# Performance work log

Hardware: AMD Instinct MI355X
Metric: run time of the kernel (lower is better)

The kernel has to match this reference:

```python
import jax, jax.numpy as jnp
import numpy as np

HIDDEN = 2048
HEADS = 16
HEAD_DIM = HIDDEN // HEADS


def setup_inputs() -> dict:
    key = jax.random.key(0)
    k1, k2, k3, k4, k5 = jax.random.split(key, 5)
    scale = 1.0 / np.sqrt(HIDDEN)
    x = jax.random.normal(k1, (2, 2048, HIDDEN), dtype=jnp.float32)
    # nn.Linear weights stored as [out_features, in_features]
    w_q = jax.random.normal(k2, (HIDDEN, HIDDEN), dtype=jnp.float32) * scale
    w_k = jax.random.normal(k3, (HEAD_DIM, HIDDEN), dtype=jnp.float32) * scale
    w_v = jax.random.normal(k4, (HEAD_DIM, HIDDEN), dtype=jnp.float32) * scale
    w_out = jax.random.normal(k5, (HIDDEN, HIDDEN), dtype=jnp.float32) * scale
    return {"x": x, "w_q": w_q, "w_k": w_k, "w_v": w_v, "w_out": w_out}


def reference(x, w_q, w_k, w_v, w_out) -> jnp.ndarray:
    bsz, seq_len, _ = x.shape
    norm = jnp.asarray(np.sqrt(HEAD_DIM), dtype=x.dtype)
    # projections (Linear: x @ W^T)
    q = (x @ w_q.T).reshape(bsz, seq_len, HEADS, HEAD_DIM)  # [b,s,h,d]
    k = x @ w_k.T  # [b,s,d] single shared KV head
    v = x @ w_v.T  # [b,s,d]
    # attention scores: [b,h,s,s], K/V broadcast across heads
    att = jnp.einsum("bshd,btd->bhst", q, k) / norm
    att = jax.nn.softmax(att, axis=-1)
    out = jnp.einsum("bhst,btd->bshd", att, v).reshape(bsz, seq_len, HIDDEN)
    return out @ w_out.T
```

## Files before the change

kernel.cpp:

```cpp
#include <hip/hip_runtime.h>


using bf16   = __bf16;
using bf16x2 = __bf16 __attribute__((ext_vector_type(2)));
using bf16x4 = __bf16 __attribute__((ext_vector_type(4)));
using bf16x8 = __bf16 __attribute__((ext_vector_type(8)));
using f32x4  = float  __attribute__((ext_vector_type(4)));
using u32x4  = unsigned __attribute__((ext_vector_type(4)));

#define GAS __attribute__((address_space(1)))
#define LAS __attribute__((address_space(3)))

__device__ __forceinline__ void load_lds16(const bf16* g, bf16* l) {
    __builtin_amdgcn_global_load_lds((const GAS void*)g, (LAS void*)l, 16, 0, 0);
}

__device__ __forceinline__ unsigned pkbf(float a, float b) {
    bf16x2 t; t[0] = (bf16)a; t[1] = (bf16)b;
    return __builtin_bit_cast(unsigned, t);
}
__device__ __forceinline__ void perm32(unsigned& a, unsigned& b) {
    asm volatile("v_permlane32_swap_b32 %0, %1" : "+v"(a), "+v"(b));
}
__device__ __forceinline__ void perm16(unsigned& a, unsigned& b) {
    asm volatile("v_permlane16_swap_b32 %0, %1" : "+v"(a), "+v"(b));
}

#define Q_SCALE_LOG2 0.12751745f

__global__ __launch_bounds__(256) void cvt_all(
    const float* __restrict__ x,  const float* __restrict__ wq,
    const float* __restrict__ wk, const float* __restrict__ wv,
    const float* __restrict__ wo, bf16* __restrict__ dst)
{
    const size_t i = (size_t)(blockIdx.x * 256 + threadIdx.x) * 8;
    const float* src; size_t off;
    if      (i <  8388608) { src = x;  off = 0; }
    else if (i < 12582912) { src = wq; off = 8388608; }
    else if (i < 12845056) { src = wk; off = 12582912; }
    else if (i < 13107200) { src = wv; off = 12845056; }
    else                   { src = wo; off = 13107200; }
    float4 f0 = *(const float4*)(src + (i - off));
    float4 f1 = *(const float4*)(src + (i - off) + 4);
    bf16x8 v;
    v[0] = (bf16)f0.x; v[1] = (bf16)f0.y; v[2] = (bf16)f0.z; v[3] = (bf16)f0.w;
    v[4] = (bf16)f1.x; v[5] = (bf16)f1.y; v[6] = (bf16)f1.z; v[7] = (bf16)f1.w;
    *(bf16x8*)(dst + i) = v;
}

__device__ __forceinline__ void gemm128(
    const bf16* __restrict__ A, const bf16* __restrict__ B, void* __restrict__ Cp,
    int bm, int bn, int ldC, int mode, float scale)
{
    __shared__ bf16 As[128 * 32];
    __shared__ bf16 Bs[128 * 32];
    const int K = 2048;

    const int tid  = threadIdx.x;
    const int wave = tid >> 6;
    const int lane = tid & 63;
    const int quad = lane >> 4;
    const int c    = lane & 15;
    const int wm   = (wave >> 1) << 6;
    const int wn   = (wave & 1) << 6;

    const int srow = tid >> 2;
    const int scol = (tid & 3) << 3;
    const bf16* Ag = A + (size_t)(bm + srow) * K + scol;
    const bf16* Bg = B + (size_t)(bn + srow) * K + scol;
    bf16* lA = As + wave * 512;
    bf16* lB = Bs + wave * 512;

    f32x4 acc[4][4];
#pragma unroll
    for (int i = 0; i < 4; ++i)
#pragma unroll
        for (int j = 0; j < 4; ++j)
            acc[i][j] = f32x4{0.f, 0.f, 0.f, 0.f};

    for (int k0 = 0; k0 < K; k0 += 32) {
        load_lds16(Ag + k0,          lA);
        load_lds16(Ag + k0 + 64 * K, lA + 2048);
        load_lds16(Bg + k0,          lB);
        load_lds16(Bg + k0 + 64 * K, lB + 2048);
        __syncthreads();

        bf16x8 af[4], bfv[4];
#pragma unroll
        for (int i = 0; i < 4; ++i)
            af[i] = *(const bf16x8*)(As + (wm + i * 16 + c) * 32 + quad * 8);
#pragma unroll
        for (int j = 0; j < 4; ++j)
            bfv[j] = *(const bf16x8*)(Bs + (wn + j * 16 + c) * 32 + quad * 8);
#pragma unroll
        for (int i = 0; i < 4; ++i)
#pragma unroll
            for (int j = 0; j < 4; ++j)
                acc[i][j] = __builtin_amdgcn_mfma_f32_16x16x32_bf16(af[i], bfv[j], acc[i][j], 0, 0, 0);
        __syncthreads();
    }

    if (mode == 0) {
        bf16* C = (bf16*)Cp;
#pragma unroll
        for (int i = 0; i < 4; ++i) {
            const int m = bm + wm + i * 16 + quad * 4;
#pragma unroll
            for (int j = 0; j < 4; ++j) {
                const int n = bn + wn + j * 16 + c;
#pragma unroll
                for (int r = 0; r < 4; ++r)
                    C[(size_t)(m + r) * ldC + n] = (bf16)(acc[i][j][r] * scale);
            }
        }
    } else if (mode == 1) {
        bf16* C = (bf16*)Cp;
#pragma unroll
        for (int j = 0; j < 4; ++j) {
            const int n = bn + wn + j * 16 + c;
#pragma unroll
            for (int i = 0; i < 4; ++i) {
                const int m = bm + wm + i * 16 + quad * 4;
                bf16x4 v;
#pragma unroll
                for (int r = 0; r < 4; ++r) v[r] = (bf16)acc[i][j][r];
                *(bf16x4*)(C + (size_t)n * ldC + m) = v;
            }
        }
    } else {
        float* C = (float*)Cp;
#pragma unroll
        for (int i = 0; i < 4; ++i) {
            const int m = bm + wm + i * 16 + quad * 4;
#pragma unroll
            for (int j = 0; j < 4; ++j) {
                const int n = bn + wn + j * 16 + c;
#pragma unroll
                for (int r = 0; r < 4; ++r)
                    C[(size_t)(m + r) * ldC + n] = acc[i][j][r];
            }
        }
    }
}

__global__ __launch_bounds__(256, 3) void qkv_kernel(
    const bf16* __restrict__ x,  const bf16* __restrict__ wq,
    const bf16* __restrict__ wk, const bf16* __restrict__ wv,
    bf16* __restrict__ Qb, bf16* __restrict__ Kb, bf16* __restrict__ Vt)
{
    const int bx = blockIdx.x;
    const int bm = blockIdx.y << 7;
    const bf16* B; bf16* C; int ldC, bn, mode; float sc;
    if (bx < 16)       { B = wq; C = Qb; ldC = 2048; bn = bx << 7; mode = 0; sc = Q_SCALE_LOG2; }
    else if (bx == 16) { B = wk; C = Kb; ldC = 128;  bn = 0;       mode = 0; sc = 1.0f; }
    else               { B = wv; C = Vt; ldC = 4096; bn = 0;       mode = 1; sc = 1.0f; }
    gemm128(x, B, C, bm, bn, ldC, mode, sc);
}

__global__ __launch_bounds__(256, 3) void out_kernel(
    const bf16* __restrict__ AO, const bf16* __restrict__ wo, float* __restrict__ out)
{
    gemm128(AO, wo, out, blockIdx.y << 7, blockIdx.x << 7, 2048, 2, 1.0f);
}

#define KS_LD 136
#define VS_LD 72

__global__ __launch_bounds__(256, 2) void attn_kernel(
    const bf16* __restrict__ Qb, const bf16* __restrict__ Kb,
    const bf16* __restrict__ Vt, bf16* __restrict__ AO)
{
    __shared__ bf16 Ks[64 * KS_LD];
    __shared__ bf16 Vs[128 * VS_LD];

    const int tid  = threadIdx.x;
    const int lane = tid & 63;
    const int wave = tid >> 6;
    const int q    = lane >> 4;
    const int c    = lane & 15;
    const int qt = blockIdx.x, h = blockIdx.y, b = blockIdx.z;
    const int rowbase = b * 2048 + qt * 128;
    const int wrow = wave * 32;

    bf16x8 qf[2][4];
#pragma unroll
    for (int nq = 0; nq < 2; ++nq)
#pragma unroll
        for (int ks = 0; ks < 4; ++ks)
            qf[nq][ks] = *(const bf16x8*)(Qb + (size_t)(rowbase + wrow + nq * 16 + c) * 2048
                                             + h * 128 + ks * 32 + q * 8);

    f32x4 o[8][2];
#pragma unroll
    for (int mtv = 0; mtv < 8; ++mtv)
#pragma unroll
        for (int nq = 0; nq < 2; ++nq) o[mtv][nq] = f32x4{0.f, 0.f, 0.f, 0.f};

    float psum[2] = {0.f, 0.f};

    const int krow = tid >> 4, kcol = (tid & 15) << 3;
    const int vrow = tid >> 3, vcol = (tid & 7) << 3;
    const bf16* Kg = Kb + (size_t)b * 2048 * 128;
    const bf16* Vg = Vt + (size_t)b * 2048;

    for (int t0 = 0; t0 < 2048; t0 += 64) {
        bf16x8 kreg[4], vreg[4];
#pragma unroll
        for (int p = 0; p < 4; ++p)
            kreg[p] = *(const bf16x8*)(Kg + (size_t)(t0 + p * 16 + krow) * 128 + kcol);
#pragma unroll
        for (int p = 0; p < 4; ++p)
            vreg[p] = *(const bf16x8*)(Vg + (size_t)(p * 32 + vrow) * 4096 + t0 + vcol);

        __syncthreads();
#pragma unroll
        for (int p = 0; p < 4; ++p)
            *(bf16x8*)(Ks + (p * 16 + krow) * KS_LD + kcol) = kreg[p];
#pragma unroll
        for (int p = 0; p < 4; ++p)
            *(bf16x8*)(Vs + (p * 32 + vrow) * VS_LD + vcol) = vreg[p];
        __syncthreads();

        f32x4 s[4][2];
#pragma unroll
        for (int mt = 0; mt < 4; ++mt)
#pragma unroll
            for (int nq = 0; nq < 2; ++nq) s[mt][nq] = f32x4{0.f, 0.f, 0.f, 0.f};
#pragma unroll
        for (int ks = 0; ks < 4; ++ks) {
            bf16x8 kf[4];
#pragma unroll
            for (int mt = 0; mt < 4; ++mt)
                kf[mt] = *(const bf16x8*)(Ks + (mt * 16 + c) * KS_LD + ks * 32 + q * 8);
#pragma unroll
            for (int mt = 0; mt < 4; ++mt)
#pragma unroll
                for (int nq = 0; nq < 2; ++nq)
                    s[mt][nq] = __builtin_amdgcn_mfma_f32_16x16x32_bf16(kf[mt], qf[nq][ks], s[mt][nq], 0, 0, 0);
        }

        float p[4][2][4];
#pragma unroll
        for (int mt = 0; mt < 4; ++mt)
#pragma unroll
            for (int nq = 0; nq < 2; ++nq)
#pragma unroll
                for (int r = 0; r < 4; ++r) {
                    const float e = exp2f(s[mt][nq][r]);
                    p[mt][nq][r] = e;
                    psum[nq] += e;
                }

#pragma unroll
        for (int j = 0; j < 2; ++j) {
            bf16x8 vb[8];
#pragma unroll
            for (int mtv = 0; mtv < 8; ++mtv)
                vb[mtv] = *(const bf16x8*)(Vs + (mtv * 16 + c) * VS_LD + j * 32 + q * 8);
#pragma unroll
            for (int nq = 0; nq < 2; ++nq) {
                unsigned a0 = pkbf(p[2 * j][nq][0],     p[2 * j][nq][1]);
                unsigned a1 = pkbf(p[2 * j][nq][2],     p[2 * j][nq][3]);
                unsigned b0 = pkbf(p[2 * j + 1][nq][0], p[2 * j + 1][nq][1]);
                unsigned b1 = pkbf(p[2 * j + 1][nq][2], p[2 * j + 1][nq][3]);
                perm32(a0, b0); perm32(a1, b1);
                perm16(a0, b0); perm16(a1, b1);
                const bf16x8 pf = __builtin_bit_cast(bf16x8, u32x4{a0, a1, b0, b1});
#pragma unroll
                for (int mtv = 0; mtv < 8; ++mtv)
                    o[mtv][nq] = __builtin_amdgcn_mfma_f32_16x16x32_bf16(vb[mtv], pf, o[mtv][nq], 0, 0, 0);
            }
        }
    }

#pragma unroll
    for (int nq = 0; nq < 2; ++nq) {
        float v = psum[nq];
        v += __shfl_xor(v, 16);
        v += __shfl_xor(v, 32);
        psum[nq] = v;
    }

#pragma unroll
    for (int nq = 0; nq < 2; ++nq) {
        const float rinv = 1.0f / psum[nq];
        const size_t row = (size_t)(rowbase + wrow + nq * 16 + c) * 2048 + h * 128;
#pragma unroll
        for (int mtv = 0; mtv < 8; ++mtv) {
            bf16x4 v;
#pragma unroll
            for (int r = 0; r < 4; ++r) v[r] = (bf16)(o[mtv][nq][r] * rinv);
            *(bf16x4*)(AO + row + mtv * 16 + q * 4) = v;
        }
    }
}

extern "C" void kernel_launch(void* const* d_in, const int* in_sizes, int n_in,
                              void* d_out, int out_size, void* d_ws, size_t ws_size,
                              hipStream_t stream)
{
    const float* x  = (const float*)d_in[0];
    const float* wq = (const float*)d_in[1];
    const float* wk = (const float*)d_in[2];
    const float* wv = (const float*)d_in[3];
    const float* wo = (const float*)d_in[4];
    float* out = (float*)d_out;

    char* ws = (char*)d_ws;
    const size_t MB = 1024 * 1024;
    bf16* xb  = (bf16*)(ws);
    bf16* wqb = (bf16*)(ws + 16 * MB);
    bf16* wkb = (bf16*)(ws + 24 * MB);
    bf16* wvb = (bf16*)(ws + 24 * MB + 512 * 1024);
    bf16* wob = (bf16*)(ws + 25 * MB);
    bf16* Qb  = (bf16*)(ws + 33 * MB);
    bf16* AO  = Qb;
    bf16* Kb  = (bf16*)(ws + 49 * MB);
    bf16* Vt  = (bf16*)(ws + 50 * MB);

    cvt_all<<<17301504 / 2048, 256, 0, stream>>>(x, wq, wk, wv, wo, xb);
    qkv_kernel<<<dim3(18, 32), 256, 0, stream>>>(xb, wqb, wkb, wvb, Qb, Kb, Vt);
    attn_kernel<<<dim3(16, 16, 2), 256, 0, stream>>>(Qb, Kb, Vt, AO);
    out_kernel<<<dim3(16, 32), 256, 0, stream>>>(AO, wob, out);
}
```

Baseline: 292.6 us.

## Double-buffer K/V tiles in LDS with register prefetch in attention kernel

Result: slower. 482.3 us (+64.8%).

```diff
diff --git a/kernel.cpp b/kernel.cpp
--- a/kernel.cpp
+++ b/kernel.cpp
@@ -163,15 +163,15 @@
     gemm128(AO, wo, out, blockIdx.y << 7, blockIdx.x << 7, 2048, 2, 1.0f);
 }
 
-#define KS_LD 136
-#define VS_LD 72
+#define KS_LD 130
+#define VS_LD 66
 
 __global__ __launch_bounds__(256, 2) void attn_kernel(
     const bf16* __restrict__ Qb, const bf16* __restrict__ Kb,
     const bf16* __restrict__ Vt, bf16* __restrict__ AO)
 {
-    __shared__ bf16 Ks[64 * KS_LD];
-    __shared__ bf16 Vs[128 * VS_LD];
+    __shared__ bf16 Ks[2][64 * KS_LD];
+    __shared__ bf16 Vs[2][128 * VS_LD];
 
     const int tid  = threadIdx.x;
     const int lane = tid & 63;
@@ -203,41 +203,56 @@
     const bf16* Kg = Kb + (size_t)b * 2048 * 128;
     const bf16* Vg = Vt + (size_t)b * 2048;
 
+    bf16x8 kreg[4], vreg[4];
+#pragma unroll
+    for (int p = 0; p < 4; ++p)
+        kreg[p] = *(const bf16x8*)(Kg + (size_t)(p * 16 + krow) * 128 + kcol);
+#pragma unroll
+    for (int p = 0; p < 4; ++p)
+        vreg[p] = *(const bf16x8*)(Vg + (size_t)(p * 32 + vrow) * 4096 + vcol);
+#pragma unroll
+    for (int p = 0; p < 4; ++p)
+        *(bf16x8*)(&Ks[0][0] + (p * 16 + krow) * KS_LD + kcol) = kreg[p];
+#pragma unroll
+    for (int p = 0; p < 4; ++p)
+        *(bf16x8*)(&Vs[0][0] + (p * 32 + vrow) * VS_LD + vcol) = vreg[p];
+    __syncthreads();
+
     for (int t0 = 0; t0 < 2048; t0 += 64) {
-        bf16x8 kreg[4], vreg[4];
-#pragma unroll
-        for (int p = 0; p < 4; ++p)
-            kreg[p] = *(const bf16x8*)(Kg + (size_t)(t0 + p * 16 + krow) * 128 + kcol);
-#pragma unroll
-        for (int p = 0; p < 4; ++p)
-            vreg[p] = *(const bf16x8*)(Vg + (size_t)(p * 32 + vrow) * 4096 + t0 + vcol);
-
-        __syncthreads();
-#pragma unroll
-        for (int p = 0; p < 4; ++p)
-            *(bf16x8*)(Ks + (p * 16 + krow) * KS_LD + kcol) = kreg[p];
-#pragma unroll
-        for (int p = 0; p < 4; ++p)
-            *(bf16x8*)(Vs + (p * 32 + vrow) * VS_LD + vcol) = vreg[p];
-        __syncthreads();
+        const int buf = (t0 >> 6) & 1;
+        const bool has_next = (t0 + 64) < 2048;
+        const bf16* ks_ = &Ks[buf][0];
+        const bf16* vs_ = &Vs[buf][0];
+
+        if (has_next) {
+            const int tn = t0 + 64;
+#pragma unroll
+            for (int p = 0; p < 4; ++p)
+                kreg[p] = *(const bf16x8*)(Kg + (size_t)(tn + p * 16 + krow) * 128 + kcol);
+#pragma unroll
+            for (int p = 0; p < 4; ++p)
+                vreg[p] = *(const bf16x8*)(Vg + (size_t)(p * 32 + vrow) * 4096 + tn + vcol);
+        }
 
         f32x4 s[4][2];
 #pragma unroll
         for (int mt = 0; mt < 4; ++mt)
 #pragma unroll
             for (int nq = 0; nq < 2; ++nq) s[mt][nq] = f32x4{0.f, 0.f, 0.f, 0.f};
+        __builtin_amdgcn_s_setprio(1);
 #pragma unroll
         for (int ks = 0; ks < 4; ++ks) {
             bf16x8 kf[4];
 #pragma unroll
             for (int mt = 0; mt < 4; ++mt)
-                kf[mt] = *(const bf16x8*)(Ks + (mt * 16 + c) * KS_LD + ks * 32 + q * 8);
+                kf[mt] = *(const bf16x8*)(ks_ + (mt * 16 + c) * KS_LD + ks * 32 + q * 8);
 #pragma unroll
             for (int mt = 0; mt < 4; ++mt)
 #pragma unroll
                 for (int nq = 0; nq < 2; ++nq)
                     s[mt][nq] = __builtin_amdgcn_mfma_f32_16x16x32_bf16(kf[mt], qf[nq][ks], s[mt][nq], 0, 0, 0);
         }
+        __builtin_amdgcn_s_setprio(0);
 
         float p[4][2][4];
 #pragma unroll
@@ -246,7 +261,7 @@
             for (int nq = 0; nq < 2; ++nq)
 #pragma unroll
                 for (int r = 0; r < 4; ++r) {
-                    const float e = exp2f(s[mt][nq][r]);
+                    const float e = __builtin_amdgcn_exp2f(s[mt][nq][r]);
                     p[mt][nq][r] = e;
                     psum[nq] += e;
                 }
@@ -256,7 +271,7 @@
             bf16x8 vb[8];
 #pragma unroll
             for (int mtv = 0; mtv < 8; ++mtv)
-                vb[mtv] = *(const bf16x8*)(Vs + (mtv * 16 + c) * VS_LD + j * 32 + q * 8);
+                vb[mtv] = *(const bf16x8*)(vs_ + (mtv * 16 + c) * VS_LD + j * 32 + q * 8);
 #pragma unroll
             for (int nq = 0; nq < 2; ++nq) {
                 unsigned a0 = pkbf(p[2 * j][nq][0],     p[2 * j][nq][1]);
@@ -266,10 +281,24 @@
                 perm32(a0, b0); perm32(a1, b1);
                 perm16(a0, b0); perm16(a1, b1);
                 const bf16x8 pf = __builtin_bit_cast(bf16x8, u32x4{a0, a1, b0, b1});
+                __builtin_amdgcn_s_setprio(1);
 #pragma unroll
                 for (int mtv = 0; mtv < 8; ++mtv)
                     o[mtv][nq] = __builtin_amdgcn_mfma_f32_16x16x32_bf16(vb[mtv], pf, o[mtv][nq], 0, 0, 0);
+                __builtin_amdgcn_s_setprio(0);
             }
+        }
+
+        if (has_next) {
+            bf16* kd = &Ks[buf ^ 1][0];
+            bf16* vd = &Vs[buf ^ 1][0];
+#pragma unroll
+            for (int p = 0; p < 4; ++p)
+                *(bf16x8*)(kd + (p * 16 + krow) * KS_LD + kcol) = kreg[p];
+#pragma unroll
+            for (int p = 0; p < 4; ++p)
+                *(bf16x8*)(vd + (p * 32 + vrow) * VS_LD + vcol) = vreg[p];
+            __syncthreads();
         }
     }
 
```

## Split attention key range into two chunks and merge partial outputs

Applied to the files above, without the earlier changes.

Result: slower. 379.5 us (+29.7%).

```diff
diff --git a/kernel.cpp b/kernel.cpp
--- a/kernel.cpp
+++ b/kernel.cpp
@@ -166,9 +166,10 @@
 #define KS_LD 136
 #define VS_LD 72
 
-__global__ __launch_bounds__(256, 2) void attn_kernel(
+__global__ __launch_bounds__(256, 4) void attn_kernel(
     const bf16* __restrict__ Qb, const bf16* __restrict__ Kb,
-    const bf16* __restrict__ Vt, bf16* __restrict__ AO)
+    const bf16* __restrict__ Vt, bf16* __restrict__ P0,
+    bf16* __restrict__ P1, float* __restrict__ Lp)
 {
     __shared__ bf16 Ks[64 * KS_LD];
     __shared__ bf16 Vs[128 * VS_LD];
@@ -178,9 +179,12 @@
     const int wave = tid >> 6;
     const int q    = lane >> 4;
     const int c    = lane & 15;
-    const int qt = blockIdx.x, h = blockIdx.y, b = blockIdx.z;
+    const int qt = blockIdx.x, h = blockIdx.y;
+    const int b = blockIdx.z & 1, chunk = blockIdx.z >> 1;
+    const int tbeg = chunk << 10;
     const int rowbase = b * 2048 + qt * 128;
     const int wrow = wave * 32;
+    bf16* Pout = chunk ? P1 : P0;
 
     bf16x8 qf[2][4];
 #pragma unroll
@@ -203,7 +207,7 @@
     const bf16* Kg = Kb + (size_t)b * 2048 * 128;
     const bf16* Vg = Vt + (size_t)b * 2048;
 
-    for (int t0 = 0; t0 < 2048; t0 += 64) {
+    for (int t0 = tbeg; t0 < tbeg + 1024; t0 += 64) {
         bf16x8 kreg[4], vreg[4];
 #pragma unroll
         for (int p = 0; p < 4; ++p)
@@ -246,7 +250,7 @@
             for (int nq = 0; nq < 2; ++nq)
 #pragma unroll
                 for (int r = 0; r < 4; ++r) {
-                    const float e = exp2f(s[mt][nq][r]);
+                    const float e = __builtin_amdgcn_exp2f(s[mt][nq][r]);
                     p[mt][nq][r] = e;
                     psum[nq] += e;
                 }
@@ -290,9 +294,33 @@
             bf16x4 v;
 #pragma unroll
             for (int r = 0; r < 4; ++r) v[r] = (bf16)(o[mtv][nq][r] * rinv);
-            *(bf16x4*)(AO + row + mtv * 16 + q * 4) = v;
-        }
-    }
+            *(bf16x4*)(Pout + row + mtv * 16 + q * 4) = v;
+        }
+        if (q == 0)
+            Lp[((size_t)((chunk * 2 + b) * 16 + h)) * 2048 + qt * 128 + wrow + nq * 16 + c] = psum[nq];
+    }
+}
+
+__global__ __launch_bounds__(256) void merge_kernel(
+    const bf16* __restrict__ P0, const bf16* __restrict__ P1,
+    const float* __restrict__ Lp, bf16* __restrict__ AO)
+{
+    const int row = blockIdx.x;
+    const int t = threadIdx.x;
+    const int h = t >> 4;
+    const int b = row >> 11, qrow = row & 2047;
+    const float l1 = Lp[(size_t)(b * 16 + h) * 2048 + qrow];
+    const float l2 = Lp[(size_t)((2 + b) * 16 + h) * 2048 + qrow];
+    const float w1 = l1 / (l1 + l2);
+    const float w2 = 1.0f - w1;
+    const size_t off = (size_t)row * 2048 + t * 8;
+    const bf16x8 a = *(const bf16x8*)(P0 + off);
+    const bf16x8 bb = *(const bf16x8*)(P1 + off);
+    bf16x8 ov;
+#pragma unroll
+    for (int r = 0; r < 8; ++r)
+        ov[r] = (bf16)((float)a[r] * w1 + (float)bb[r] * w2);
+    *(bf16x8*)(AO + off) = ov;
 }
 
 extern "C" void kernel_launch(void* const* d_in, const int* in_sizes, int n_in,
@@ -317,9 +345,13 @@
     bf16* AO  = Qb;
     bf16* Kb  = (bf16*)(ws + 49 * MB);
     bf16* Vt  = (bf16*)(ws + 50 * MB);
+    bf16* P0  = (bf16*)(ws);
+    bf16* P1  = (bf16*)d_out;
+    float* Lp = (float*)(ws + 16 * MB);
 
     cvt_all<<<17301504 / 2048, 256, 0, stream>>>(x, wq, wk, wv, wo, xb);
     qkv_kernel<<<dim3(18, 32), 256, 0, stream>>>(xb, wqb, wkb, wvb, Qb, Kb, Vt);
-    attn_kernel<<<dim3(16, 16, 2), 256, 0, stream>>>(Qb, Kb, Vt, AO);
+    attn_kernel<<<dim3(16, 16, 4), 256, 0, stream>>>(Qb, Kb, Vt, P0, P1, Lp);
+    merge_kernel<<<4096, 256, 0, stream>>>(P0, P1, Lp, AO);
     out_kernel<<<dim3(16, 32), 256, 0, stream>>>(AO, wob, out);
 }
```
